# Kernel optimization log

Hardware: AMD Instinct MI355X
Metric: run time of the kernel (lower is better)

The kernel has to match this reference:

```python
import jax, jax.numpy as jnp
import numpy as np

BATCH, IN_DIM, HID, OUT_DIM, Z = 8192, 2048, 4096, 2048, 4
CONN_P = 0.5  # Bernoulli keep-probability y


def random_activation(h, ids):
    # ids: [dim] int32 in [0,5); per-channel nonlinearity applied over batch.
    ids = ids[None, :]
    return jnp.select(
        [ids == 0, ids == 1, ids == 2, ids == 3],
        [jax.nn.relu(h), jax.nn.sigmoid(h), jnp.tanh(h), jnp.where(h >= 0, h, 0.1 * h)],
        jax.nn.selu(h),
    )


def _make_linear(key, fan_in, fan_out):
    kw, kb, km = jax.random.split(key, 3)
    w = jax.random.normal(kw, (fan_out, fan_in), dtype=jnp.float32)
    mask = jax.random.bernoulli(km, CONN_P, (fan_out, fan_in)).astype(jnp.float32)
    b = jax.random.normal(kb, (fan_out,), dtype=jnp.float32)
    return w * mask, b


def setup_inputs() -> dict:
    key = jax.random.key(0)
    ks = jax.random.split(key, 16)
    inp = {"input_pattern": jax.random.normal(ks[0], (BATCH, IN_DIM), dtype=jnp.float32)}
    dims = [(IN_DIM, HID)] + [(HID, HID)] * Z + [(HID, OUT_DIM)]  # z+2 Linear layers
    for i, (fi, fo) in enumerate(dims):
        w, b = _make_linear(ks[1 + i], fi, fo)
        inp[f"w{i}"] = w
        inp[f"b{i}"] = b
        inp[f"ids{i}"] = jax.random.randint(ks[8 + i], (fo,), 0, 5, dtype=jnp.int32)
    return inp


def reference(input_pattern, w0, b0, ids0, w1, b1, ids1, w2, b2, ids2,
              w3, b3, ids3, w4, b4, ids4, w5, b5, ids5):
    ws = (w0, w1, w2, w3, w4, w5)
    bs = (b0, b1, b2, b3, b4, b5)
    ids = (ids0, ids1, ids2, ids3, ids4, ids5)
    h = input_pattern
    for w, b, i in zip(ws, bs, ids):
        h = random_activation(h @ w.T + b, i)
    return h
```

## Files before the change

### kernel.cpp

```cpp
#include <hip/hip_runtime.h>

typedef _Float16 f16;
typedef _Float16 f16x8 __attribute__((ext_vector_type(8)));
typedef float f32x4 __attribute__((ext_vector_type(4)));

__device__ __forceinline__ void gload_lds16(const void* g, void* l) {
  __builtin_amdgcn_global_load_lds(
      (const __attribute__((address_space(1))) void*)g,
      (__attribute__((address_space(3))) void*)l, 16, 0, 0);
}

__device__ __forceinline__ float act_apply(float x, int id) {
  switch (id) {
    case 0: return fmaxf(x, 0.0f);
    case 1: return 1.0f / (1.0f + __expf(-x));
    case 2: return tanhf(x);
    case 3: return x >= 0.0f ? x : 0.1f * x;
    default: return 1.0507009873554805f *
                    (x > 0.0f ? x : 1.6732632423543772f * expm1f(x));
  }
}

template <bool FINAL>
__global__ __launch_bounds__(512, 2)
void gemm_bias_act(const f16* __restrict__ A, const f16* __restrict__ W,
                   const float* __restrict__ bias, const int* __restrict__ ids,
                   float Sa, float invSn, void* __restrict__ outv,
                   int M, int N, int K) {
  __shared__ f16 lA[4][256 * 32];
  __shared__ f16 lB[4][256 * 32];

  const int tid  = (int)threadIdx.x;
  const int lane = tid & 63;
  const int wid  = tid >> 6;
  const int wm   = wid >> 2;
  const int wn   = wid & 3;

  const int nbx = N >> 8;
  const int nwg = (M >> 8) * nbx;
  const int b   = (int)blockIdx.x;
  const int swz = (b & 7) * (nwg >> 3) + (b >> 3);
  const int brow = (swz / nbx) << 8;
  const int bcol = (swz % nbx) << 8;

  const int d0 = tid << 4;
  const int d1 = d0 + 8192;
  const int s0 = d0 ^ (((d0 >> 7) & 7) << 4);
  const int s1 = d1 ^ (((d1 >> 7) & 7) << 4);
  const int r0 = s0 >> 6, c0 = (s0 >> 4) & 3;
  const int r1 = s1 >> 6, c1 = (s1 >> 4) & 3;

  const f16* pA0 = A + (long)(brow + r0) * K + c0 * 8;
  const f16* pA1 = A + (long)(brow + r1) * K + c1 * 8;
  const f16* pB0 = W + (long)(bcol + r0) * K + c0 * 8;
  const f16* pB1 = W + (long)(bcol + r1) * K + c1 * 8;
  const int e0 = tid << 3;
  const int e1 = e0 + 4096;

  const int fr = lane & 15;
  const int kb = lane >> 4;
  const int xorv = ((fr >> 1) & 7) << 4;
  const char* baA = (const char*)&lA[0][0];
  const char* baB = (const char*)&lB[0][0];

  int offA[8], offB[4];
#pragma unroll
  for (int m = 0; m < 8; ++m)
    offA[m] = (((wm * 128 + m * 16 + fr) << 6) + (kb << 4)) ^ xorv;
#pragma unroll
  for (int n = 0; n < 4; ++n)
    offB[n] = (((wn * 64 + n * 16 + fr) << 6) + (kb << 4)) ^ xorv;

  f32x4 acc[8][4];
#pragma unroll
  for (int m = 0; m < 8; ++m)
#pragma unroll
    for (int n = 0; n < 4; ++n) acc[m][n] = (f32x4){0.f, 0.f, 0.f, 0.f};

  const int nt = K >> 5;

#pragma unroll
  for (int t = 0; t < 3; ++t) {
    const long kk = (long)t << 5;
    gload_lds16(pA0 + kk, &lA[t][e0]);
    gload_lds16(pA1 + kk, &lA[t][e1]);
    gload_lds16(pB0 + kk, &lB[t][e0]);
    gload_lds16(pB1 + kk, &lB[t][e1]);
  }
  asm volatile("s_waitcnt vmcnt(8)" ::: "memory");
  __builtin_amdgcn_s_barrier();
  asm volatile("" ::: "memory");

  for (int s = 0; s < nt; ++s) {
    const int so  = (s & 3) << 14;
    const int ps  = (s + 3 < nt) ? (s + 3) : (nt - 1);
    const int pso = ps & 3;
    const long kk = (long)ps << 5;

    f16x8 af[4], bf[4];

#pragma unroll
    for (int m = 0; m < 4; ++m) af[m] = *(const f16x8*)(baA + so + offA[m]);
#pragma unroll
    for (int n = 0; n < 4; ++n) bf[n] = *(const f16x8*)(baB + so + offB[n]);
    gload_lds16(pA0 + kk, &lA[pso][e0]);
    gload_lds16(pA1 + kk, &lA[pso][e1]);
    if (!(s & 1)) asm volatile("s_waitcnt vmcnt(6)" ::: "memory");
    __builtin_amdgcn_s_barrier();
    asm volatile("s_waitcnt lgkmcnt(0)" ::: "memory");
    __builtin_amdgcn_sched_barrier(0);
    __builtin_amdgcn_s_setprio(1);
#pragma unroll
    for (int m = 0; m < 4; ++m)
#pragma unroll
      for (int n = 0; n < 4; ++n)
        acc[m][n] = __builtin_amdgcn_mfma_f32_16x16x32_f16(af[m], bf[n],
                                                           acc[m][n], 0, 0, 0);
    __builtin_amdgcn_s_setprio(0);
    __builtin_amdgcn_sched_barrier(0);
    __builtin_amdgcn_s_barrier();

#pragma unroll
    for (int m = 0; m < 4; ++m) af[m] = *(const f16x8*)(baA + so + offA[m + 4]);
    gload_lds16(pB0 + kk, &lB[pso][e0]);
    gload_lds16(pB1 + kk, &lB[pso][e1]);
    __builtin_amdgcn_s_barrier();
    asm volatile("s_waitcnt lgkmcnt(0)" ::: "memory");
    __builtin_amdgcn_sched_barrier(0);
    __builtin_amdgcn_s_setprio(1);
#pragma unroll
    for (int m = 0; m < 4; ++m)
#pragma unroll
      for (int n = 0; n < 4; ++n)
        acc[4 + m][n] = __builtin_amdgcn_mfma_f32_16x16x32_f16(af[m], bf[n],
                                                               acc[4 + m][n],
                                                               0, 0, 0);
    __builtin_amdgcn_s_setprio(0);
    __builtin_amdgcn_sched_barrier(0);
    __builtin_amdgcn_s_barrier();
  }
  asm volatile("s_waitcnt vmcnt(0)" ::: "memory");

  const int r4 = (lane >> 4) << 2;
#pragma unroll
  for (int n = 0; n < 4; ++n) {
    const int gcol = bcol + wn * 64 + n * 16 + fr;
    const float bv = bias[gcol];
    const int id   = ids[gcol];
#pragma unroll
    for (int m = 0; m < 8; ++m) {
      const int grow = brow + wm * 128 + m * 16 + r4;
#pragma unroll
      for (int i = 0; i < 4; ++i) {
        const float y = act_apply(acc[m][n][i] * Sa + bv, id);
        if (FINAL) {
          ((float*)outv)[(long)(grow + i) * N + gcol] = y;
        } else {
          ((f16*)outv)[(long)(grow + i) * N + gcol] = (f16)(y * invSn);
        }
      }
    }
  }
}

__global__ void cvt_f32_to_f16(const float* __restrict__ in, f16* __restrict__ out,
                               float scale, int n) {
  int i = ((int)blockIdx.x * 256 + (int)threadIdx.x) * 8;
  const int stride = (int)gridDim.x * 256 * 8;
  for (; i < n; i += stride) {
    const float4 v0 = *(const float4*)(in + i);
    const float4 v1 = *(const float4*)(in + i + 4);
    f16x8 h;
    h[0] = (f16)(v0.x * scale); h[1] = (f16)(v0.y * scale);
    h[2] = (f16)(v0.z * scale); h[3] = (f16)(v0.w * scale);
    h[4] = (f16)(v1.x * scale); h[5] = (f16)(v1.y * scale);
    h[6] = (f16)(v1.z * scale); h[7] = (f16)(v1.w * scale);
    *(f16x8*)(out + i) = h;
  }
}

extern "C" void kernel_launch(void* const* d_in, const int* in_sizes, int n_in,
                              void* d_out, int out_size, void* d_ws, size_t ws_size,
                              hipStream_t stream) {
  (void)in_sizes; (void)n_in; (void)out_size; (void)ws_size;
  const int M = 8192, IND = 2048, HID = 4096, OUTD = 2048;
  const float* x = (const float*)d_in[0];

  f16* actA = (f16*)d_ws;
  f16* actB = actA + (size_t)M * HID;
  f16* wbuf = actB + (size_t)M * HID;

  const float S[6] = {1.f, 16.f, 512.f, 16384.f, 262144.f, 8388608.f};

  const int Ks[6] = {IND, HID, HID, HID, HID, HID};
  const int Ns[6] = {HID, HID, HID, HID, HID, OUTD};

  cvt_f32_to_f16<<<2048, 256, 0, stream>>>(x, actA, 1.0f, M * IND);

  f16* cur = actA;
  f16* nxt = actB;
  for (int i = 0; i < 6; ++i) {
    const int K = Ks[i], N = Ns[i];
    const float* w  = (const float*)d_in[1 + 3 * i];
    const float* bs = (const float*)d_in[2 + 3 * i];
    const int* id   = (const int*)d_in[3 + 3 * i];

    cvt_f32_to_f16<<<2048, 256, 0, stream>>>(w, wbuf, 1.0f, N * K);

    const int nblk = (M >> 8) * (N >> 8);
    if (i < 5) {
      gemm_bias_act<false><<<nblk, 512, 0, stream>>>(
          cur, wbuf, bs, id, S[i], 1.0f / S[i + 1], nxt, M, N, K);
      f16* t = cur; cur = nxt; nxt = t;
    } else {
      gemm_bias_act<true><<<nblk, 512, 0, stream>>>(
          cur, wbuf, bs, id, S[i], 1.0f, d_out, M, N, K);
    }
  }
}
```

Measured before the change: 2.139 ms.

## Software-pipeline LDS fragment reads in 256 GEMM and add 128-tile GEMM for later layers

The 256x256 GEMM main loop is restructured to issue the LDS fragment reads for the next k-step while the current step's MFMAs run. The loop body is unrolled by two with ping-pong register sets, and global prefetches are merged so there is one wait and barrier per step. A new simpler 128x128 tile kernel with 4 waves and double-buffered LDS is added and used for layers 3 to 5. The goal is to hide LDS latency and reduce barrier count. The trade-off is higher register pressure in the 256 kernel and a less tuned pipeline in the 128 kernel.

```diff
diff --git a/kernel.cpp b/kernel.cpp
--- a/kernel.cpp
+++ b/kernel.cpp
@@ -23,10 +23,10 @@
 
 template <bool FINAL>
 __global__ __launch_bounds__(512, 2)
-void gemm_bias_act(const f16* __restrict__ A, const f16* __restrict__ W,
-                   const float* __restrict__ bias, const int* __restrict__ ids,
-                   float Sa, float invSn, void* __restrict__ outv,
-                   int M, int N, int K) {
+void gemm256(const f16* __restrict__ A, const f16* __restrict__ W,
+             const float* __restrict__ bias, const int* __restrict__ ids,
+             float Sa, float invSn, void* __restrict__ outv,
+             int M, int N, int K) {
   __shared__ f16 lA[4][256 * 32];
   __shared__ f16 lB[4][256 * 32];
 
@@ -87,58 +87,66 @@
     gload_lds16(pB0 + kk, &lB[t][e0]);
     gload_lds16(pB1 + kk, &lB[t][e1]);
   }
-  asm volatile("s_waitcnt vmcnt(8)" ::: "memory");
+  asm volatile("s_waitcnt vmcnt(4)" ::: "memory");
   __builtin_amdgcn_s_barrier();
   asm volatile("" ::: "memory");
 
-  for (int s = 0; s < nt; ++s) {
-    const int so  = (s & 3) << 14;
-    const int ps  = (s + 3 < nt) ? (s + 3) : (nt - 1);
-    const int pso = ps & 3;
-    const long kk = (long)ps << 5;
-
-    f16x8 af[4], bf[4];
-
-#pragma unroll
-    for (int m = 0; m < 4; ++m) af[m] = *(const f16x8*)(baA + so + offA[m]);
-#pragma unroll
-    for (int n = 0; n < 4; ++n) bf[n] = *(const f16x8*)(baB + so + offB[n]);
-    gload_lds16(pA0 + kk, &lA[pso][e0]);
-    gload_lds16(pA1 + kk, &lA[pso][e1]);
-    if (!(s & 1)) asm volatile("s_waitcnt vmcnt(6)" ::: "memory");
-    __builtin_amdgcn_s_barrier();
-    asm volatile("s_waitcnt lgkmcnt(0)" ::: "memory");
-    __builtin_amdgcn_sched_barrier(0);
-    __builtin_amdgcn_s_setprio(1);
-#pragma unroll
-    for (int m = 0; m < 4; ++m)
-#pragma unroll
-      for (int n = 0; n < 4; ++n)
-        acc[m][n] = __builtin_amdgcn_mfma_f32_16x16x32_f16(af[m], bf[n],
-                                                           acc[m][n], 0, 0, 0);
-    __builtin_amdgcn_s_setprio(0);
-    __builtin_amdgcn_sched_barrier(0);
-    __builtin_amdgcn_s_barrier();
-
-#pragma unroll
-    for (int m = 0; m < 4; ++m) af[m] = *(const f16x8*)(baA + so + offA[m + 4]);
-    gload_lds16(pB0 + kk, &lB[pso][e0]);
-    gload_lds16(pB1 + kk, &lB[pso][e1]);
-    __builtin_amdgcn_s_barrier();
-    asm volatile("s_waitcnt lgkmcnt(0)" ::: "memory");
-    __builtin_amdgcn_sched_barrier(0);
-    __builtin_amdgcn_s_setprio(1);
-#pragma unroll
-    for (int m = 0; m < 4; ++m)
-#pragma unroll
-      for (int n = 0; n < 4; ++n)
-        acc[4 + m][n] = __builtin_amdgcn_mfma_f32_16x16x32_f16(af[m], bf[n],
-                                                               acc[4 + m][n],
-                                                               0, 0, 0);
-    __builtin_amdgcn_s_setprio(0);
-    __builtin_amdgcn_sched_barrier(0);
-    __builtin_amdgcn_s_barrier();
-  }
+  f16x8 aC[4], bC[4], aN[4], bN[4], aL[4];
+#pragma unroll
+  for (int m = 0; m < 4; ++m) aC[m] = *(const f16x8*)(baA + offA[m]);
+#pragma unroll
+  for (int n = 0; n < 4; ++n) bC[n] = *(const f16x8*)(baB + offB[n]);
+
+#define BODY(U, AC, BC, AN, BN)                                            \
+  do {                                                                     \
+    const int so  = ((U) & 3) << 14;                                       \
+    const int son = (((U) + 1) & 3) << 14;                                 \
+    _Pragma("unroll")                                                      \
+    for (int m = 0; m < 4; ++m)                                            \
+      aL[m] = *(const f16x8*)(baA + so + offA[m + 4]);                     \
+    if ((U) + 1 < nt) {                                                    \
+      _Pragma("unroll")                                                    \
+      for (int m = 0; m < 4; ++m)                                          \
+        AN[m] = *(const f16x8*)(baA + son + offA[m]);                      \
+      _Pragma("unroll")                                                    \
+      for (int n = 0; n < 4; ++n)                                          \
+        BN[n] = *(const f16x8*)(baB + son + offB[n]);                      \
+    }                                                                      \
+    {                                                                      \
+      const int ps  = ((U) + 3 < nt) ? (U) + 3 : nt - 1;                   \
+      const int pso = ps & 3;                                              \
+      const long kk = (long)ps << 5;                                       \
+      gload_lds16(pA0 + kk, &lA[pso][e0]);                                 \
+      gload_lds16(pA1 + kk, &lA[pso][e1]);                                 \
+      gload_lds16(pB0 + kk, &lB[pso][e0]);                                 \
+      gload_lds16(pB1 + kk, &lB[pso][e1]);                                 \
+    }                                                                      \
+    __builtin_amdgcn_s_setprio(1);                                         \
+    _Pragma("unroll")                                                      \
+    for (int m = 0; m < 4; ++m)                                            \
+      _Pragma("unroll")                                                    \
+      for (int n = 0; n < 4; ++n)                                          \
+        acc[m][n] = __builtin_amdgcn_mfma_f32_16x16x32_f16(                \
+            AC[m], BC[n], acc[m][n], 0, 0, 0);                             \
+    _Pragma("unroll")                                                      \
+    for (int m = 0; m < 4; ++m)                                            \
+      _Pragma("unroll")                                                    \
+      for (int n = 0; n < 4; ++n)                                          \
+        acc[4 + m][n] = __builtin_amdgcn_mfma_f32_16x16x32_f16(            \
+            aL[m], BC[n], acc[4 + m][n], 0, 0, 0);                         \
+    __builtin_amdgcn_s_setprio(0);                                         \
+    if ((U) < nt - 1) {                                                    \
+      asm volatile("s_waitcnt vmcnt(4)" ::: "memory");                     \
+      __builtin_amdgcn_s_barrier();                                        \
+      asm volatile("" ::: "memory");                                       \
+    }                                                                      \
+  } while (0)
+
+  for (int s = 0; s < nt; s += 2) {
+    BODY(s, aC, bC, aN, bN);
+    BODY(s + 1, aN, bN, aC, bC);
+  }
+#undef BODY
   asm volatile("s_waitcnt vmcnt(0)" ::: "memory");
 
   const int r4 = (lane >> 4) << 2;
@@ -150,6 +158,118 @@
 #pragma unroll
     for (int m = 0; m < 8; ++m) {
       const int grow = brow + wm * 128 + m * 16 + r4;
+#pragma unroll
+      for (int i = 0; i < 4; ++i) {
+        const float y = act_apply(acc[m][n][i] * Sa + bv, id);
+        if (FINAL) {
+          ((float*)outv)[(long)(grow + i) * N + gcol] = y;
+        } else {
+          ((f16*)outv)[(long)(grow + i) * N + gcol] = (f16)(y * invSn);
+        }
+      }
+    }
+  }
+}
+
+template <bool FINAL>
+__global__ __launch_bounds__(256, 4)
+void gemm128(const f16* __restrict__ A, const f16* __restrict__ W,
+             const float* __restrict__ bias, const int* __restrict__ ids,
+             float Sa, float invSn, void* __restrict__ outv,
+             int M, int N, int K) {
+  __shared__ f16 lA[2][128 * 32];
+  __shared__ f16 lB[2][128 * 32];
+
+  const int tid  = (int)threadIdx.x;
+  const int lane = tid & 63;
+  const int wid  = tid >> 6;
+  const int wr   = (wid >> 1) * 64;
+  const int wc   = (wid & 1) * 64;
+
+  const int nbx = N >> 7;
+  const int nwg = (M >> 7) * nbx;
+  const int b   = (int)blockIdx.x;
+  const int swz = (b & 7) * (nwg >> 3) + (b >> 3);
+  const int brow = (swz / nbx) << 7;
+  const int bcol = (swz % nbx) << 7;
+
+  const int d0 = tid << 4;
+  const int d1 = d0 + 4096;
+  const int s0 = d0 ^ (((d0 >> 7) & 7) << 4);
+  const int s1 = d1 ^ (((d1 >> 7) & 7) << 4);
+  const int r0 = s0 >> 6, c0 = (s0 >> 4) & 3;
+  const int r1 = s1 >> 6, c1 = (s1 >> 4) & 3;
+
+  const f16* pA0 = A + (long)(brow + r0) * K + c0 * 8;
+  const f16* pA1 = A + (long)(brow + r1) * K + c1 * 8;
+  const f16* pB0 = W + (long)(bcol + r0) * K + c0 * 8;
+  const f16* pB1 = W + (long)(bcol + r1) * K + c1 * 8;
+  const int e0 = tid << 3;
+  const int e1 = e0 + 2048;
+
+  const int fr = lane & 15;
+  const int kb = lane >> 4;
+  const int xorv = ((fr >> 1) & 7) << 4;
+
+  int offA[4], offB[4];
+#pragma unroll
+  for (int m = 0; m < 4; ++m)
+    offA[m] = (((wr + m * 16 + fr) << 6) + (kb << 4)) ^ xorv;
+#pragma unroll
+  for (int n = 0; n < 4; ++n)
+    offB[n] = (((wc + n * 16 + fr) << 6) + (kb << 4)) ^ xorv;
+
+  f32x4 acc[4][4];
+#pragma unroll
+  for (int m = 0; m < 4; ++m)
+#pragma unroll
+    for (int n = 0; n < 4; ++n) acc[m][n] = (f32x4){0.f, 0.f, 0.f, 0.f};
+
+  const int nt = K >> 5;
+  int buf = 0;
+
+  gload_lds16(pA0, &lA[0][e0]);
+  gload_lds16(pA1, &lA[0][e1]);
+  gload_lds16(pB0, &lB[0][e0]);
+  gload_lds16(pB1, &lB[0][e1]);
+  __syncthreads();
+
+  for (int t = 0; t < nt; ++t) {
+    if (t + 1 < nt) {
+      const long kk = (long)(t + 1) << 5;
+      gload_lds16(pA0 + kk, &lA[buf ^ 1][e0]);
+      gload_lds16(pA1 + kk, &lA[buf ^ 1][e1]);
+      gload_lds16(pB0 + kk, &lB[buf ^ 1][e0]);
+      gload_lds16(pB1 + kk, &lB[buf ^ 1][e1]);
+    }
+    const char* bA = (const char*)&lA[buf][0];
+    const char* bB = (const char*)&lB[buf][0];
+    f16x8 af[4], bf[4];
+#pragma unroll
+    for (int m = 0; m < 4; ++m) af[m] = *(const f16x8*)(bA + offA[m]);
+#pragma unroll
+    for (int n = 0; n < 4; ++n) bf[n] = *(const f16x8*)(bB + offB[n]);
+#pragma unroll
+    for (int m = 0; m < 4; ++m)
+#pragma unroll
+      for (int n = 0; n < 4; ++n)
+        acc[m][n] = __builtin_amdgcn_mfma_f32_16x16x32_f16(af[m], bf[n],
+                                                           acc[m][n], 0, 0, 0);
+    if (t + 1 < nt) {
+      __syncthreads();
+      buf ^= 1;
+    }
+  }
+
+  const int r4 = (lane >> 4) << 2;
+#pragma unroll
+  for (int n = 0; n < 4; ++n) {
+    const int gcol = bcol + wc + n * 16 + fr;
+    const float bv = bias[gcol];
+    const int id   = ids[gcol];
+#pragma unroll
+    for (int m = 0; m < 4; ++m) {
+      const int grow = brow + wr + m * 16 + r4;
 #pragma unroll
       for (int i = 0; i < 4; ++i) {
         const float y = act_apply(acc[m][n][i] * Sa + bv, id);
@@ -191,7 +311,6 @@
   f16* wbuf = actB + (size_t)M * HID;
 
   const float S[6] = {1.f, 16.f, 512.f, 16384.f, 262144.f, 8388608.f};
-
   const int Ks[6] = {IND, HID, HID, HID, HID, HID};
   const int Ns[6] = {HID, HID, HID, HID, HID, OUTD};
 
@@ -207,13 +326,19 @@
 
     cvt_f32_to_f16<<<2048, 256, 0, stream>>>(w, wbuf, 1.0f, N * K);
 
-    const int nblk = (M >> 8) * (N >> 8);
-    if (i < 5) {
-      gemm_bias_act<false><<<nblk, 512, 0, stream>>>(
+    if (i < 3) {
+      const int nblk = (M >> 8) * (N >> 8);
+      gemm256<false><<<nblk, 512, 0, stream>>>(
+          cur, wbuf, bs, id, S[i], 1.0f / S[i + 1], nxt, M, N, K);
+      f16* t = cur; cur = nxt; nxt = t;
+    } else if (i < 5) {
+      const int nblk = (M >> 7) * (N >> 7);
+      gemm128<false><<<nblk, 256, 0, stream>>>(
           cur, wbuf, bs, id, S[i], 1.0f / S[i + 1], nxt, M, N, K);
       f16* t = cur; cur = nxt; nxt = t;
     } else {
-      gemm_bias_act<true><<<nblk, 512, 0, stream>>>(
+      const int nblk = (M >> 7) * (N >> 7);
+      gemm128<true><<<nblk, 256, 0, stream>>>(
           cur, wbuf, bs, id, S[i], 1.0f, d_out, M, N, K);
     }
   }
```

Result: faster. 1.943 ms (-9.2%).
